# Optimization experiments

Measured on AMD Instinct MI355X. Metric: run time of the kernel, lower is better.

## Reference

```python
import jax, jax.numpy as jnp
import numpy as np

N_IN = 100000
N_OUT = 50000
K = 32
E = N_OUT * K
CIN = 16
COUT = 32
KS = 4  # kernel_size per axis


def setup_inputs() -> dict:
    key = jax.random.key(0)
    ks = jax.random.split(key, 8)
    feats = jax.random.normal(ks[0], (N_IN, CIN), jnp.float32)
    inp_points = jax.random.uniform(ks[1], (N_IN, 3), jnp.float32)
    out_points = jax.random.uniform(ks[2], (N_OUT, 3), jnp.float32)
    # voxel size (extent) per output point
    out_extents = 0.1 + 0.1 * jax.random.uniform(ks[3], (N_OUT,), jnp.float32)
    scale_compat = jax.random.uniform(ks[4], (E,), jnp.float32)
    neighbors_index = jax.random.randint(ks[5], (E,), 0, N_IN, jnp.int32)
    # fixed-degree ragged structure: K neighbors per output voxel
    neighbors_row_splits = (jnp.arange(N_OUT + 1) * K).astype(jnp.int32)
    neighbors_distance = jax.random.uniform(ks[6], (E,), jnp.float32)
    kernel = 0.1 * jax.random.normal(ks[7], (KS, KS, KS, CIN, COUT), jnp.float32)
    bias = 0.01 * jax.random.normal(jax.random.fold_in(key, 99), (COUT,), jnp.float32)
    return dict(feats=feats, inp_points=inp_points, out_points=out_points,
                out_extents=out_extents, scale_compat=scale_compat,
                neighbors_index=neighbors_index,
                neighbors_row_splits=neighbors_row_splits,
                neighbors_distance=neighbors_distance, kernel=kernel, bias=bias)


def window_poly6(d):
    # poly6 smoothing window on normalized distance, clamped to [0,1]
    return jnp.clip((1.0 - d * d) ** 3, 0.0, 1.0)


def reference(feats, inp_points, out_points, out_extents, scale_compat,
              neighbors_index, neighbors_row_splits, neighbors_distance,
              kernel, bias):
    E_ = neighbors_index.shape[0]
    n_out = out_points.shape[0]
    cin = feats.shape[1]
    cout = kernel.shape[-1]
    nk = KS * KS * KS  # 64 kernel taps

    # per-edge output id from row_splits
    out_ids = jnp.searchsorted(neighbors_row_splits, jnp.arange(E_), side='right') - 1

    # per-neighbor importance = scale_compat * window_poly6(distance)
    imp = scale_compat * window_poly6(neighbors_distance)

    # relative position normalized to [-1,1] ball (extent is full voxel size)
    rel = (inp_points[neighbors_index] - out_points[out_ids]) / (0.5 * out_extents[out_ids])[:, None]

    # ball_to_cube_radial: radially stretch ball to cube, u = v * ||v||_2 / ||v||_inf
    r = jnp.sqrt(jnp.sum(rel * rel, axis=-1))
    linf = jnp.max(jnp.abs(rel), axis=-1)
    u = rel * (r / jnp.maximum(linf, 1e-12))[:, None]

    # trilinear interpolation coords in kernel grid [0, KS-1]
    t = jnp.clip((u * 0.5 + 0.5) * (KS - 1), 0.0, KS - 1.0)
    t0 = jnp.clip(jnp.floor(t), 0.0, KS - 2.0)
    f = t - t0                      # fractional part, [E,3]
    t0 = t0.astype(jnp.int32)

    # importance-weighted gathered features [E, Cin]
    fe = feats[neighbors_index] * imp[:, None]

    # scatter into per-output per-tap accumulator B [N_out*64, Cin]
    B = jnp.zeros((n_out * nk, cin), feats.dtype)
    for dx in (0, 1):
        wx = f[:, 0] if dx else 1.0 - f[:, 0]
        ix = t0[:, 0] + dx
        for dy in (0, 1):
            wy = f[:, 1] if dy else 1.0 - f[:, 1]
            iy = t0[:, 1] + dy
            for dz in (0, 1):
                wz = f[:, 2] if dz else 1.0 - f[:, 2]
                iz = t0[:, 2] + dz
                w = wx * wy * wz
                kflat = (ix * KS + iy) * KS + iz
                seg = out_ids * nk + kflat
                B = B + jax.ops.segment_sum(fe * w[:, None], seg, num_segments=n_out * nk)

    # contract taps with kernel: [n_out,64,cin] x [64,cin,cout] -> [n_out,cout]
    out = jnp.einsum('nkc,kcd->nd', B.reshape(n_out, nk, cin), kernel.reshape(nk, cin, cout))

    # normalize by summed importance per output point
    den = jax.ops.segment_sum(imp, out_ids, num_segments=n_out)
    out = out / jnp.where(den > 0, den, 1.0)[:, None]

    return jax.nn.relu(out + bias)
```

## Files before the change

### kernel.cpp

```cpp
#include <hip/hip_runtime.h>
#include <hip/hip_fp16.h>

#define NOUT 50000
#define KNB 32
#define CIN 16
#define COUT 32
#define NTAP 64
#define GP 8
#define ROW2B 2064

typedef __attribute__((ext_vector_type(8))) _Float16 half8;
typedef __attribute__((ext_vector_type(2))) _Float16 h2v;
typedef __attribute__((ext_vector_type(4))) float f32x4;

__device__ __forceinline__ h2v pmax(h2v a, h2v b) {
  h2v d;
  asm("v_pk_max_f16 %0, %1, %2" : "=v"(d) : "v"(a), "v"(b));
  return d;
}
__device__ __forceinline__ unsigned int pkh(float lo, float hi) {
  union { __half2 h; unsigned int u; } cv;
  cv.h = __floats2half2_rn(lo, hi);
  return cv.u;
}
__device__ __forceinline__ unsigned short f2hbits(float f) {
  union { __half h; unsigned short s; } c; c.h = __float2half_rn(f); return c.s;
}

__global__ void prep_w_kernel(const float* __restrict__ kern,
                              unsigned short* __restrict__ wf) {
  int idx = blockIdx.x * 256 + threadIdx.x;
  if (idx >= NTAP * CIN * COUT) return;
  int j = idx & 7;
  int n = (idx >> 3) & 31;
  int g = (idx >> 8) & 3;
  int s = idx >> 10;
  int kc = s * 32 + g * 8 + j;
  wf[idx] = f2hbits(kern[kc * COUT + n]);
}

__launch_bounds__(256, 8)
__global__ void cconv_kernel(const float* __restrict__ feats,
                             const float* __restrict__ inp_points,
                             const float* __restrict__ out_points,
                             const float* __restrict__ out_extents,
                             const float* __restrict__ scale_compat,
                             const int* __restrict__ nidx,
                             const float* __restrict__ ndist,
                             const unsigned short* __restrict__ wf,
                             const float* __restrict__ bias,
                             float* __restrict__ out) {
  __shared__ __align__(16) char s_bl[GP * ROW2B];
  __shared__ __align__(4) unsigned short s_tx[GP * KNB];
  __shared__ __align__(4) unsigned short s_ty[GP * KNB];
  __shared__ __align__(4) unsigned short s_tz[GP * KNB];
  __shared__ __align__(4) unsigned short s_im[GP * KNB];
  __shared__ float s_cacc[GP][COUT];
  __shared__ float s_den[GP];

  const int tid = threadIdx.x;
  const int wv = tid >> 6;
  const int lane = tid & 63;
  const int c = lane & 15;
  const int g = lane >> 4;

  ((float*)s_cacc)[tid] = 0.0f;

  const int my_nb = nidx[blockIdx.x * (GP * KNB) + tid];
  float fpre[2][8];
#pragma unroll
  for (int h = 0; h < 2; ++h) {
#pragma unroll
    for (int j = 0; j < 8; ++j) {
      const int nb = __shfl(my_nb, h * 32 + g * 8 + j);
      fpre[h][j] = feats[nb * CIN + c];
    }
  }

  {
    const int h = lane >> 5;
    const int e = lane & 31;
    const int p = wv * 2 + h;
    const int pg = blockIdx.x * GP + p;
    const int eg = pg * KNB + e;
    const int nb = my_nb;
    const float d = ndist[eg];
    float q = 1.0f - d * d;
    float w6 = q * q * q;
    w6 = fminf(fmaxf(w6, 0.0f), 1.0f);
    const float imp = scale_compat[eg] * w6;

    const float inv = 1.0f / (0.5f * out_extents[pg]);
    const float rx = (inp_points[nb * 3 + 0] - out_points[pg * 3 + 0]) * inv;
    const float ry = (inp_points[nb * 3 + 1] - out_points[pg * 3 + 1]) * inv;
    const float rz = (inp_points[nb * 3 + 2] - out_points[pg * 3 + 2]) * inv;
    const float r = sqrtf(rx * rx + ry * ry + rz * rz);
    const float linf = fmaxf(fabsf(rx), fmaxf(fabsf(ry), fabsf(rz)));
    const float sf = r / fmaxf(linf, 1e-12f);
    const float tx = fminf(fmaxf((rx * sf * 0.5f + 0.5f) * 3.0f, 0.0f), 3.0f);
    const float ty = fminf(fmaxf((ry * sf * 0.5f + 0.5f) * 3.0f, 0.0f), 3.0f);
    const float tz = fminf(fmaxf((rz * sf * 0.5f + 0.5f) * 3.0f, 0.0f), 3.0f);

    s_tx[tid] = f2hbits(tx);
    s_ty[tid] = f2hbits(ty);
    s_tz[tid] = f2hbits(tz);
    s_im[tid] = f2hbits(imp);

    float dsum = imp;
#pragma unroll
    for (int m = 1; m < 32; m <<= 1) dsum += __shfl_xor(dsum, m);
    if (e == 0) s_den[p] = dsum;
  }

  {
    const _Float16 kys = (_Float16)(short)(c >> 2);
    const _Float16 kzs = (_Float16)(short)(c & 3);
    const h2v z2 = {(_Float16)0, (_Float16)0};
    const h2v one2 = {(_Float16)1, (_Float16)1};
    const h2v two2 = {(_Float16)2, (_Float16)2};
    const h2v ky2 = {kys, kys};
    const h2v kz2 = {kzs, kzs};
#pragma unroll
    for (int h = 0; h < 2; ++h) {
      const int p = wv * 2 + h;
      union { unsigned int u[4]; h2v h[4]; half8 v; } wfr0, wfr1, wfr2, wfr3, fef;
#pragma unroll
      for (int jp = 0; jp < 4; ++jp) {
        const int eb = p * KNB + g * 8 + jp * 2;
        const h2v tx2 = *(const h2v*)&s_tx[eb];
        const h2v ty2 = *(const h2v*)&s_ty[eb];
        const h2v tz2 = *(const h2v*)&s_tz[eb];
        const h2v im2 = *(const h2v*)&s_im[eb];
        h2v t = ty2 - ky2;
        h2v at = pmax(t, z2 - t);
        const h2v hy = pmax(z2, one2 - at);
        t = tz2 - kz2;
        at = pmax(t, z2 - t);
        const h2v hz = pmax(z2, one2 - at);
        const h2v m2 = hy * hz * im2;
        const h2v w0 = pmax(z2, one2 - tx2) * m2;
        t = tx2 - one2;
        at = pmax(t, z2 - t);
        const h2v w1 = pmax(z2, one2 - at) * m2;
        t = tx2 - two2;
        at = pmax(t, z2 - t);
        const h2v w2 = pmax(z2, one2 - at) * m2;
        const h2v w3 = pmax(z2, t) * m2;
        wfr0.h[jp] = w0;
        wfr1.h[jp] = w1;
        wfr2.h[jp] = w2;
        wfr3.h[jp] = w3;
        fef.u[jp] = pkh(fpre[h][jp * 2], fpre[h][jp * 2 + 1]);
      }
      const f32x4 z = {0.f, 0.f, 0.f, 0.f};
      f32x4 d0 = __builtin_amdgcn_mfma_f32_16x16x32_f16(fef.v, wfr0.v, z, 0, 0, 0);
      f32x4 d1 = __builtin_amdgcn_mfma_f32_16x16x32_f16(fef.v, wfr1.v, z, 0, 0, 0);
      f32x4 d2 = __builtin_amdgcn_mfma_f32_16x16x32_f16(fef.v, wfr2.v, z, 0, 0, 0);
      f32x4 d3 = __builtin_amdgcn_mfma_f32_16x16x32_f16(fef.v, wfr3.v, z, 0, 0, 0);
      char* bp = s_bl + (unsigned)(p * ROW2B + c * 32 + g * 8);
      *(uint2*)(bp + 0 * 512) = make_uint2(pkh(d0[0], d0[1]), pkh(d0[2], d0[3]));
      *(uint2*)(bp + 1 * 512) = make_uint2(pkh(d1[0], d1[1]), pkh(d1[2], d1[3]));
      *(uint2*)(bp + 2 * 512) = make_uint2(pkh(d2[0], d2[1]), pkh(d2[2], d2[3]));
      *(uint2*)(bp + 3 * 512) = make_uint2(pkh(d3[0], d3[1]), pkh(d3[2], d3[3]));
    }
  }

  __syncthreads();

  f32x4 acc0 = {0.f, 0.f, 0.f, 0.f}, acc1 = {0.f, 0.f, 0.f, 0.f};
  const int pl = lane & 15;
  const int arow = pl & (GP - 1);
  const int g4 = lane >> 4;
#pragma unroll
  for (int ss = 0; ss < 8; ++ss) {
    const int s = wv * 8 + ss;
    const half8 a = *(const half8*)(s_bl + arow * ROW2B + s * 64 + g4 * 16);
    const half8 b0 = *(const half8*)(wf + ((unsigned)((s * 4 + g4) * 32) + pl) * 8);
    const half8 b1 = *(const half8*)(wf + ((unsigned)((s * 4 + g4) * 32) + 16 + pl) * 8);
    acc0 = __builtin_amdgcn_mfma_f32_16x16x32_f16(a, b0, acc0, 0, 0, 0);
    acc1 = __builtin_amdgcn_mfma_f32_16x16x32_f16(a, b1, acc1, 0, 0, 0);
  }
#pragma unroll
  for (int j = 0; j < 4; ++j) {
    const int row = g4 * 4 + j;
    if (row < GP) {
      atomicAdd(&s_cacc[row][pl], acc0[j]);
      atomicAdd(&s_cacc[row][pl + 16], acc1[j]);
    }
  }

  __syncthreads();

  {
    const int p = tid >> 5;
    const int dch = tid & 31;
    const float den = s_den[p];
    float v = ((float*)s_cacc)[tid] / (den > 0.0f ? den : 1.0f) + bias[dch];
    out[blockIdx.x * (GP * COUT) + tid] = fmaxf(v, 0.0f);
  }
}

extern "C" void kernel_launch(void* const* d_in, const int* in_sizes, int n_in,
                              void* d_out, int out_size, void* d_ws, size_t ws_size,
                              hipStream_t stream) {
  const float* feats        = (const float*)d_in[0];
  const float* inp_points   = (const float*)d_in[1];
  const float* out_points   = (const float*)d_in[2];
  const float* out_extents  = (const float*)d_in[3];
  const float* scale_compat = (const float*)d_in[4];
  const int*   nidx         = (const int*)d_in[5];
  const float* ndist        = (const float*)d_in[7];
  const float* kern         = (const float*)d_in[8];
  const float* bias         = (const float*)d_in[9];
  unsigned short* wf = (unsigned short*)d_ws;

  prep_w_kernel<<<(NTAP * CIN * COUT + 255) / 256, 256, 0, stream>>>(kern, wf);
  cconv_kernel<<<NOUT / GP, 256, 0, stream>>>(feats, inp_points, out_points,
                                              out_extents, scale_compat, nidx,
                                              ndist, wf, bias, (float*)d_out);
}
```

Before: 68.96 us.

## Persistent grid with software-pipelined neighbor gathers and fp16 feature copy

Converts the main kernel into a persistent loop over 2048 blocks, each processing several output tiles and prefetching the next tile's neighbor indices, features and positions into registers while the current tile computes. The prep kernel now also converts feats to fp16 in workspace, halving gather bytes. Launch bounds drop to 7 waves per SIMD to make room for the extra prefetch registers. In exchange it adds an extra conversion pass over feats and lowers occupancy.

Result: slower. 117.9 us (+71.0%).

```diff
diff --git a/kernel.cpp b/kernel.cpp
--- a/kernel.cpp
+++ b/kernel.cpp
@@ -1,13 +1,16 @@
 #include <hip/hip_runtime.h>
 #include <hip/hip_fp16.h>
 
+#define NIN 100000
 #define NOUT 50000
 #define KNB 32
 #define CIN 16
 #define COUT 32
-#define NTAP 64
 #define GP 8
 #define ROW2B 2064
+#define WFOFF 65536
+#define NTILES (NOUT / GP)
+#define PBLK 2048
 
 typedef __attribute__((ext_vector_type(8))) _Float16 half8;
 typedef __attribute__((ext_vector_type(2))) _Float16 h2v;
@@ -27,20 +30,27 @@
   union { __half h; unsigned short s; } c; c.h = __float2half_rn(f); return c.s;
 }
 
-__global__ void prep_w_kernel(const float* __restrict__ kern,
-                              unsigned short* __restrict__ wf) {
-  int idx = blockIdx.x * 256 + threadIdx.x;
-  if (idx >= NTAP * CIN * COUT) return;
-  int j = idx & 7;
-  int n = (idx >> 3) & 31;
-  int g = (idx >> 8) & 3;
-  int s = idx >> 10;
-  int kc = s * 32 + g * 8 + j;
-  wf[idx] = f2hbits(kern[kc * COUT + n]);
-}
-
-__launch_bounds__(256, 8)
-__global__ void cconv_kernel(const float* __restrict__ feats,
+__global__ void prep_kernel(const float* __restrict__ kern,
+                            const float* __restrict__ feats,
+                            unsigned short* __restrict__ wf,
+                            unsigned short* __restrict__ f16) {
+  const int b = blockIdx.x;
+  if (b < 128) {
+    int idx = b * 256 + threadIdx.x;
+    int j = idx & 7;
+    int n = (idx >> 3) & 31;
+    int g = (idx >> 8) & 3;
+    int s = idx >> 10;
+    int kc = s * 32 + g * 8 + j;
+    wf[idx] = f2hbits(kern[kc * COUT + n]);
+  } else {
+    int idx = (b - 128) * 256 + threadIdx.x;
+    f16[idx] = f2hbits(feats[idx]);
+  }
+}
+
+__launch_bounds__(256, 7)
+__global__ void cconv_kernel(const unsigned short* __restrict__ feats16,
                              const float* __restrict__ inp_points,
                              const float* __restrict__ out_points,
                              const float* __restrict__ out_extents,
@@ -63,140 +73,210 @@
   const int lane = tid & 63;
   const int c = lane & 15;
   const int g = lane >> 4;
+  const int h1 = lane >> 5;
+  const int e1 = lane & 31;
 
   ((float*)s_cacc)[tid] = 0.0f;
 
-  const int my_nb = nidx[blockIdx.x * (GP * KNB) + tid];
-  float fpre[2][8];
-#pragma unroll
-  for (int h = 0; h < 2; ++h) {
-#pragma unroll
-    for (int j = 0; j < 8; ++j) {
-      const int nb = __shfl(my_nb, h * 32 + g * 8 + j);
-      fpre[h][j] = feats[nb * CIN + c];
-    }
+  int tile = blockIdx.x;
+
+  int nbA; float dA, scA;
+  unsigned short fpA0, fpA1, fpA2, fpA3, fpA4, fpA5, fpA6, fpA7;
+  unsigned short fpA8, fpA9, fpA10, fpA11, fpA12, fpA13, fpA14, fpA15;
+  float pxA, pyA, pzA, oxA, oyA, ozA, invA;
+  {
+    const int e0 = tile * (GP * KNB) + tid;
+    nbA = nidx[e0];
+    dA = ndist[e0];
+    scA = scale_compat[e0];
+#define GATHER_F(dst, hh, jj)                                         \
+    { const int nb_ = __shfl(nbA, (hh) * 32 + g * 8 + (jj));          \
+      dst = feats16[nb_ * CIN + c]; }
+    GATHER_F(fpA0, 0, 0) GATHER_F(fpA1, 0, 1) GATHER_F(fpA2, 0, 2) GATHER_F(fpA3, 0, 3)
+    GATHER_F(fpA4, 0, 4) GATHER_F(fpA5, 0, 5) GATHER_F(fpA6, 0, 6) GATHER_F(fpA7, 0, 7)
+    GATHER_F(fpA8, 1, 0) GATHER_F(fpA9, 1, 1) GATHER_F(fpA10, 1, 2) GATHER_F(fpA11, 1, 3)
+    GATHER_F(fpA12, 1, 4) GATHER_F(fpA13, 1, 5) GATHER_F(fpA14, 1, 6) GATHER_F(fpA15, 1, 7)
+#undef GATHER_F
+    const int pg = tile * GP + wv * 2 + h1;
+    pxA = inp_points[nbA * 3 + 0];
+    pyA = inp_points[nbA * 3 + 1];
+    pzA = inp_points[nbA * 3 + 2];
+    oxA = out_points[pg * 3 + 0];
+    oyA = out_points[pg * 3 + 1];
+    ozA = out_points[pg * 3 + 2];
+    invA = 1.0f / (0.5f * out_extents[pg]);
   }
 
-  {
-    const int h = lane >> 5;
-    const int e = lane & 31;
-    const int p = wv * 2 + h;
-    const int pg = blockIdx.x * GP + p;
-    const int eg = pg * KNB + e;
-    const int nb = my_nb;
-    const float d = ndist[eg];
-    float q = 1.0f - d * d;
-    float w6 = q * q * q;
-    w6 = fminf(fmaxf(w6, 0.0f), 1.0f);
-    const float imp = scale_compat[eg] * w6;
-
-    const float inv = 1.0f / (0.5f * out_extents[pg]);
-    const float rx = (inp_points[nb * 3 + 0] - out_points[pg * 3 + 0]) * inv;
-    const float ry = (inp_points[nb * 3 + 1] - out_points[pg * 3 + 1]) * inv;
-    const float rz = (inp_points[nb * 3 + 2] - out_points[pg * 3 + 2]) * inv;
-    const float r = sqrtf(rx * rx + ry * ry + rz * rz);
-    const float linf = fmaxf(fabsf(rx), fmaxf(fabsf(ry), fabsf(rz)));
-    const float sf = r / fmaxf(linf, 1e-12f);
-    const float tx = fminf(fmaxf((rx * sf * 0.5f + 0.5f) * 3.0f, 0.0f), 3.0f);
-    const float ty = fminf(fmaxf((ry * sf * 0.5f + 0.5f) * 3.0f, 0.0f), 3.0f);
-    const float tz = fminf(fmaxf((rz * sf * 0.5f + 0.5f) * 3.0f, 0.0f), 3.0f);
-
-    s_tx[tid] = f2hbits(tx);
-    s_ty[tid] = f2hbits(ty);
-    s_tz[tid] = f2hbits(tz);
-    s_im[tid] = f2hbits(imp);
-
-    float dsum = imp;
-#pragma unroll
-    for (int m = 1; m < 32; m <<= 1) dsum += __shfl_xor(dsum, m);
-    if (e == 0) s_den[p] = dsum;
-  }
-
-  {
-    const _Float16 kys = (_Float16)(short)(c >> 2);
-    const _Float16 kzs = (_Float16)(short)(c & 3);
-    const h2v z2 = {(_Float16)0, (_Float16)0};
-    const h2v one2 = {(_Float16)1, (_Float16)1};
-    const h2v two2 = {(_Float16)2, (_Float16)2};
-    const h2v ky2 = {kys, kys};
-    const h2v kz2 = {kzs, kzs};
-#pragma unroll
-    for (int h = 0; h < 2; ++h) {
-      const int p = wv * 2 + h;
-      union { unsigned int u[4]; h2v h[4]; half8 v; } wfr0, wfr1, wfr2, wfr3, fef;
-#pragma unroll
-      for (int jp = 0; jp < 4; ++jp) {
-        const int eb = p * KNB + g * 8 + jp * 2;
-        const h2v tx2 = *(const h2v*)&s_tx[eb];
-        const h2v ty2 = *(const h2v*)&s_ty[eb];
-        const h2v tz2 = *(const h2v*)&s_tz[eb];
-        const h2v im2 = *(const h2v*)&s_im[eb];
-        h2v t = ty2 - ky2;
-        h2v at = pmax(t, z2 - t);
-        const h2v hy = pmax(z2, one2 - at);
-        t = tz2 - kz2;
-        at = pmax(t, z2 - t);
-        const h2v hz = pmax(z2, one2 - at);
-        const h2v m2 = hy * hz * im2;
-        const h2v w0 = pmax(z2, one2 - tx2) * m2;
-        t = tx2 - one2;
-        at = pmax(t, z2 - t);
-        const h2v w1 = pmax(z2, one2 - at) * m2;
-        t = tx2 - two2;
-        at = pmax(t, z2 - t);
-        const h2v w2 = pmax(z2, one2 - at) * m2;
-        const h2v w3 = pmax(z2, t) * m2;
-        wfr0.h[jp] = w0;
-        wfr1.h[jp] = w1;
-        wfr2.h[jp] = w2;
-        wfr3.h[jp] = w3;
-        fef.u[jp] = pkh(fpre[h][jp * 2], fpre[h][jp * 2 + 1]);
+  while (true) {
+    const int tnext = tile + PBLK;
+    const bool hasN = tnext < NTILES;
+
+    int nbB = 0; float dB = 0.f, scB = 0.f;
+    if (hasN) {
+      const int e0 = tnext * (GP * KNB) + tid;
+      nbB = nidx[e0];
+      dB = ndist[e0];
+      scB = scale_compat[e0];
+    }
+
+    {
+      float q = 1.0f - dA * dA;
+      float w6 = q * q * q;
+      w6 = fminf(fmaxf(w6, 0.0f), 1.0f);
+      const float imp = scA * w6;
+      const float rx = (pxA - oxA) * invA;
+      const float ry = (pyA - oyA) * invA;
+      const float rz = (pzA - ozA) * invA;
+      const float r = sqrtf(rx * rx + ry * ry + rz * rz);
+      const float linf = fmaxf(fabsf(rx), fmaxf(fabsf(ry), fabsf(rz)));
+      const float sf = r / fmaxf(linf, 1e-12f);
+      const float tx = fminf(fmaxf((rx * sf * 0.5f + 0.5f) * 3.0f, 0.0f), 3.0f);
+      const float ty = fminf(fmaxf((ry * sf * 0.5f + 0.5f) * 3.0f, 0.0f), 3.0f);
+      const float tz = fminf(fmaxf((rz * sf * 0.5f + 0.5f) * 3.0f, 0.0f), 3.0f);
+
+      s_tx[tid] = f2hbits(tx);
+      s_ty[tid] = f2hbits(ty);
+      s_tz[tid] = f2hbits(tz);
+      s_im[tid] = f2hbits(imp);
+
+      float dsum = imp;
+#pragma unroll
+      for (int m = 1; m < 32; m <<= 1) dsum += __shfl_xor(dsum, m);
+      if (e1 == 0) s_den[wv * 2 + h1] = dsum;
+    }
+
+    {
+      const _Float16 kys = (_Float16)(short)(c >> 2);
+      const _Float16 kzs = (_Float16)(short)(c & 3);
+      const h2v z2 = {(_Float16)0, (_Float16)0};
+      const h2v one2 = {(_Float16)1, (_Float16)1};
+      const h2v two2 = {(_Float16)2, (_Float16)2};
+      const h2v ky2 = {kys, kys};
+      const h2v kz2 = {kzs, kzs};
+#pragma unroll
+      for (int h = 0; h < 2; ++h) {
+        const int p = wv * 2 + h;
+        union { unsigned int u[4]; h2v h[4]; half8 v; } wfr0, wfr1, wfr2, wfr3, fef;
+#pragma unroll
+        for (int jp = 0; jp < 4; ++jp) {
+          const int eb = p * KNB + g * 8 + jp * 2;
+          const h2v tx2 = *(const h2v*)&s_tx[eb];
+          const h2v ty2 = *(const h2v*)&s_ty[eb];
+          const h2v tz2 = *(const h2v*)&s_tz[eb];
+          const h2v im2 = *(const h2v*)&s_im[eb];
+          h2v t = ty2 - ky2;
+          h2v at = pmax(t, z2 - t);
+          const h2v hy = pmax(z2, one2 - at);
+          t = tz2 - kz2;
+          at = pmax(t, z2 - t);
+          const h2v hz = pmax(z2, one2 - at);
+          const h2v m2 = hy * hz * im2;
+          const h2v w0 = pmax(z2, one2 - tx2) * m2;
+          t = tx2 - one2;
+          at = pmax(t, z2 - t);
+          const h2v w1 = pmax(z2, one2 - at) * m2;
+          t = tx2 - two2;
+          at = pmax(t, z2 - t);
+          const h2v w2 = pmax(z2, one2 - at) * m2;
+          const h2v w3 = pmax(z2, t) * m2;
+          wfr0.h[jp] = w0;
+          wfr1.h[jp] = w1;
+          wfr2.h[jp] = w2;
+          wfr3.h[jp] = w3;
+        }
+        if (h == 0) {
+          fef.u[0] = (unsigned)fpA0 | ((unsigned)fpA1 << 16);
+          fef.u[1] = (unsigned)fpA2 | ((unsigned)fpA3 << 16);
+          fef.u[2] = (unsigned)fpA4 | ((unsigned)fpA5 << 16);
+          fef.u[3] = (unsigned)fpA6 | ((unsigned)fpA7 << 16);
+        } else {
+          fef.u[0] = (unsigned)fpA8 | ((unsigned)fpA9 << 16);
+          fef.u[1] = (unsigned)fpA10 | ((unsigned)fpA11 << 16);
+          fef.u[2] = (unsigned)fpA12 | ((unsigned)fpA13 << 16);
+          fef.u[3] = (unsigned)fpA14 | ((unsigned)fpA15 << 16);
+        }
+        const f32x4 z = {0.f, 0.f, 0.f, 0.f};
+        f32x4 d0 = __builtin_amdgcn_mfma_f32_16x16x32_f16(fef.v, wfr0.v, z, 0, 0, 0);
+        f32x4 d1 = __builtin_amdgcn_mfma_f32_16x16x32_f16(fef.v, wfr1.v, z, 0, 0, 0);
+        f32x4 d2 = __builtin_amdgcn_mfma_f32_16x16x32_f16(fef.v, wfr2.v, z, 0, 0, 0);
+        f32x4 d3 = __builtin_amdgcn_mfma_f32_16x16x32_f16(fef.v, wfr3.v, z, 0, 0, 0);
+        char* bp = s_bl + (unsigned)(p * ROW2B + c * 32 + g * 8);
+        *(uint2*)(bp + 0 * 512) = make_uint2(pkh(d0[0], d0[1]), pkh(d0[2], d0[3]));
+        *(uint2*)(bp + 1 * 512) = make_uint2(pkh(d1[0], d1[1]), pkh(d1[2], d1[3]));
+        *(uint2*)(bp + 2 * 512) = make_uint2(pkh(d2[0], d2[1]), pkh(d2[2], d2[3]));
+        *(uint2*)(bp + 3 * 512) = make_uint2(pkh(d3[0], d3[1]), pkh(d3[2], d3[3]));
       }
-      const f32x4 z = {0.f, 0.f, 0.f, 0.f};
-      f32x4 d0 = __builtin_amdgcn_mfma_f32_16x16x32_f16(fef.v, wfr0.v, z, 0, 0, 0);
-      f32x4 d1 = __builtin_amdgcn_mfma_f32_16x16x32_f16(fef.v, wfr1.v, z, 0, 0, 0);
-      f32x4 d2 = __builtin_amdgcn_mfma_f32_16x16x32_f16(fef.v, wfr2.v, z, 0, 0, 0);
-      f32x4 d3 = __builtin_amdgcn_mfma_f32_16x16x32_f16(fef.v, wfr3.v, z, 0, 0, 0);
-      char* bp = s_bl + (unsigned)(p * ROW2B + c * 32 + g * 8);
-      *(uint2*)(bp + 0 * 512) = make_uint2(pkh(d0[0], d0[1]), pkh(d0[2], d0[3]));
-      *(uint2*)(bp + 1 * 512) = make_uint2(pkh(d1[0], d1[1]), pkh(d1[2], d1[3]));
-      *(uint2*)(bp + 2 * 512) = make_uint2(pkh(d2[0], d2[1]), pkh(d2[2], d2[3]));
-      *(uint2*)(bp + 3 * 512) = make_uint2(pkh(d3[0], d3[1]), pkh(d3[2], d3[3]));
-    }
-  }
-
-  __syncthreads();
-
-  f32x4 acc0 = {0.f, 0.f, 0.f, 0.f}, acc1 = {0.f, 0.f, 0.f, 0.f};
-  const int pl = lane & 15;
-  const int arow = pl & (GP - 1);
-  const int g4 = lane >> 4;
-#pragma unroll
-  for (int ss = 0; ss < 8; ++ss) {
-    const int s = wv * 8 + ss;
-    const half8 a = *(const half8*)(s_bl + arow * ROW2B + s * 64 + g4 * 16);
-    const half8 b0 = *(const half8*)(wf + ((unsigned)((s * 4 + g4) * 32) + pl) * 8);
-    const half8 b1 = *(const half8*)(wf + ((unsigned)((s * 4 + g4) * 32) + 16 + pl) * 8);
-    acc0 = __builtin_amdgcn_mfma_f32_16x16x32_f16(a, b0, acc0, 0, 0, 0);
-    acc1 = __builtin_amdgcn_mfma_f32_16x16x32_f16(a, b1, acc1, 0, 0, 0);
-  }
-#pragma unroll
-  for (int j = 0; j < 4; ++j) {
-    const int row = g4 * 4 + j;
-    if (row < GP) {
-      atomicAdd(&s_cacc[row][pl], acc0[j]);
-      atomicAdd(&s_cacc[row][pl + 16], acc1[j]);
-    }
-  }
-
-  __syncthreads();
-
-  {
-    const int p = tid >> 5;
-    const int dch = tid & 31;
-    const float den = s_den[p];
-    float v = ((float*)s_cacc)[tid] / (den > 0.0f ? den : 1.0f) + bias[dch];
-    out[blockIdx.x * (GP * COUT) + tid] = fmaxf(v, 0.0f);
+    }
+
+    unsigned short fpB0 = 0, fpB1 = 0, fpB2 = 0, fpB3 = 0, fpB4 = 0, fpB5 = 0,
+                   fpB6 = 0, fpB7 = 0, fpB8 = 0, fpB9 = 0, fpB10 = 0, fpB11 = 0,
+                   fpB12 = 0, fpB13 = 0, fpB14 = 0, fpB15 = 0;
+    float pxB = 0, pyB = 0, pzB = 0, oxB = 0, oyB = 0, ozB = 0, invB = 0;
+    if (hasN) {
+#define GATHER_F(dst, hh, jj)                                         \
+      { const int nb_ = __shfl(nbB, (hh) * 32 + g * 8 + (jj));        \
+        dst = feats16[nb_ * CIN + c]; }
+      GATHER_F(fpB0, 0, 0) GATHER_F(fpB1, 0, 1) GATHER_F(fpB2, 0, 2) GATHER_F(fpB3, 0, 3)
+      GATHER_F(fpB4, 0, 4) GATHER_F(fpB5, 0, 5) GATHER_F(fpB6, 0, 6) GATHER_F(fpB7, 0, 7)
+      GATHER_F(fpB8, 1, 0) GATHER_F(fpB9, 1, 1) GATHER_F(fpB10, 1, 2) GATHER_F(fpB11, 1, 3)
+      GATHER_F(fpB12, 1, 4) GATHER_F(fpB13, 1, 5) GATHER_F(fpB14, 1, 6) GATHER_F(fpB15, 1, 7)
+#undef GATHER_F
+      const int pg = tnext * GP + wv * 2 + h1;
+      pxB = inp_points[nbB * 3 + 0];
+      pyB = inp_points[nbB * 3 + 1];
+      pzB = inp_points[nbB * 3 + 2];
+      oxB = out_points[pg * 3 + 0];
+      oyB = out_points[pg * 3 + 1];
+      ozB = out_points[pg * 3 + 2];
+      invB = 1.0f / (0.5f * out_extents[pg]);
+    }
+
+    __syncthreads();
+
+    f32x4 acc0 = {0.f, 0.f, 0.f, 0.f}, acc1 = {0.f, 0.f, 0.f, 0.f};
+    const int pl = lane & 15;
+    const int arow = pl & (GP - 1);
+    const int g4 = lane >> 4;
+#pragma unroll
+    for (int ss = 0; ss < 8; ++ss) {
+      const int s = wv * 8 + ss;
+      const half8 a = *(const half8*)(s_bl + arow * ROW2B + s * 64 + g4 * 16);
+      const half8 b0 = *(const half8*)(wf + ((unsigned)((s * 4 + g4) * 32) + pl) * 8);
+      const half8 b1 = *(const half8*)(wf + ((unsigned)((s * 4 + g4) * 32) + 16 + pl) * 8);
+      acc0 = __builtin_amdgcn_mfma_f32_16x16x32_f16(a, b0, acc0, 0, 0, 0);
+      acc1 = __builtin_amdgcn_mfma_f32_16x16x32_f16(a, b1, acc1, 0, 0, 0);
+    }
+#pragma unroll
+    for (int j = 0; j < 4; ++j) {
+      const int row = g4 * 4 + j;
+      if (row < GP) {
+        atomicAdd(&s_cacc[row][pl], acc0[j]);
+        atomicAdd(&s_cacc[row][pl + 16], acc1[j]);
+      }
+    }
+
+    __syncthreads();
+
+    {
+      const int p = tid >> 5;
+      const int dch = tid & 31;
+      const float den = s_den[p];
+      float v = ((float*)s_cacc)[tid] / (den > 0.0f ? den : 1.0f) + bias[dch];
+      out[tile * (GP * COUT) + tid] = fmaxf(v, 0.0f);
+      ((float*)s_cacc)[tid] = 0.0f;
+    }
+
+    if (!hasN) break;
+    __syncthreads();
+
+    tile = tnext;
+    nbA = nbB; dA = dB; scA = scB;
+    fpA0 = fpB0; fpA1 = fpB1; fpA2 = fpB2; fpA3 = fpB3;
+    fpA4 = fpB4; fpA5 = fpB5; fpA6 = fpB6; fpA7 = fpB7;
+    fpA8 = fpB8; fpA9 = fpB9; fpA10 = fpB10; fpA11 = fpB11;
+    fpA12 = fpB12; fpA13 = fpB13; fpA14 = fpB14; fpA15 = fpB15;
+    pxA = pxB; pyA = pyB; pzA = pzB;
+    oxA = oxB; oyA = oyB; ozA = ozB; invA = invB;
   }
 }
 
@@ -212,10 +292,11 @@
   const float* ndist        = (const float*)d_in[7];
   const float* kern         = (const float*)d_in[8];
   const float* bias         = (const float*)d_in[9];
-  unsigned short* wf = (unsigned short*)d_ws;
-
-  prep_w_kernel<<<(NTAP * CIN * COUT + 255) / 256, 256, 0, stream>>>(kern, wf);
-  cconv_kernel<<<NOUT / GP, 256, 0, stream>>>(feats, inp_points, out_points,
-                                              out_extents, scale_compat, nidx,
-                                              ndist, wf, bias, (float*)d_out);
-}
+  unsigned short* wf  = (unsigned short*)d_ws;
+  unsigned short* f16 = (unsigned short*)((char*)d_ws + WFOFF);
+
+  prep_kernel<<<128 + (NIN * CIN) / 256, 256, 0, stream>>>(kern, feats, wf, f16);
+  cconv_kernel<<<PBLK, 256, 0, stream>>>(f16, inp_points, out_points,
+                                         out_extents, scale_compat, nidx,
+                                         ndist, wf, bias, (float*)d_out);
+}
```
